# Kernel tuning notes

Hardware: AMD Instinct MI355X
Metric: run time of the kernel (lower is better)

The kernel has to match this reference:

```python
import jax, jax.numpy as jnp
import numpy as np

NQ = 4          # QUANTUM_QUBITS
DIM = 2 ** NQ   # 16-dim statevector
N_LAYERS = 2
BATCH = 1 << 20


def _bit(idx, w):
    # PennyLane convention: wire 0 is the most-significant bit
    return (idx >> (NQ - 1 - w)) & 1

# Precompute CNOT permutations for the ring (w, (w+1)%NQ): flip target bit when control bit is 1.
_CNOT_PERMS = []
for w in range(NQ):
    c, t = w, (w + 1) % NQ
    perm = np.arange(DIM)
    for idx in range(DIM):
        if _bit(idx, c):
            perm[idx] = idx ^ (1 << (NQ - 1 - t))
    _CNOT_PERMS.append(jnp.asarray(perm))

# Z expectation sign vectors: sign = +1 if bit==0 else -1, per wire -> (NQ, DIM)
_Z_SIGNS = jnp.asarray(
    np.stack([[1.0 - 2.0 * _bit(idx, w) for idx in range(DIM)] for w in range(NQ)]),
    dtype=jnp.float32,
)


def _ry(t):
    c, s = jnp.cos(t / 2), jnp.sin(t / 2)
    return jnp.stack([jnp.stack([c, -s], -1), jnp.stack([s, c], -1)], -2).astype(jnp.complex64)


def _rx(t):
    c = jnp.cos(t / 2).astype(jnp.complex64)
    s = (-1j * jnp.sin(t / 2)).astype(jnp.complex64)
    return jnp.stack([jnp.stack([c, s], -1), jnp.stack([s, c], -1)], -2)


def _rz(t):
    em = jnp.exp(-0.5j * t.astype(jnp.complex64))
    ep = jnp.exp(0.5j * t.astype(jnp.complex64))
    zero = jnp.zeros_like(em)
    return jnp.stack([jnp.stack([em, zero], -1), jnp.stack([zero, ep], -1)], -2)


def _apply_batched(state, g, w):
    # state: (B, DIM); g: (B, 2, 2) per-sample gate on wire w
    s = state.reshape((-1,) + (2,) * NQ)
    s = jnp.moveaxis(s, 1 + w, 1)
    s = jnp.einsum('bij,bj...->bi...', g, s)
    s = jnp.moveaxis(s, 1, 1 + w)
    return s.reshape(-1, DIM)


def _apply_shared(state, g, w):
    # state: (B, DIM); g: (2, 2) shared gate on wire w
    s = state.reshape((-1,) + (2,) * NQ)
    s = jnp.moveaxis(s, 1 + w, 1)
    s = jnp.einsum('ij,bj...->bi...', g, s)
    s = jnp.moveaxis(s, 1, 1 + w)
    return s.reshape(-1, DIM)


def setup_inputs() -> dict:
    key = jax.random.key(0)
    kx, kw = jax.random.split(key)
    x = jax.random.normal(kx, (BATCH, NQ), dtype=jnp.float32)
    weights = jax.random.normal(kw, (N_LAYERS, NQ, 3), dtype=jnp.float32) * 0.1
    return {"x": x, "weights": weights}


def reference(x, weights):
    B = x.shape[0]
    state = jnp.zeros((B, DIM), dtype=jnp.complex64).at[:, 0].set(1.0)
    # Angle embedding: RY(x_w) on each wire (per-sample gates)
    for w in range(NQ):
        state = _apply_batched(state, _ry(x[:, w]), w)
    # Variational layers: RX, RY, RZ per wire, then CNOT ring
    for l in range(weights.shape[0]):
        for w in range(NQ):
            state = _apply_shared(state, _rx(weights[l, w, 0]), w)
            state = _apply_shared(state, _ry(weights[l, w, 1]), w)
            state = _apply_shared(state, _rz(weights[l, w, 2]), w)
        for w in range(NQ):
            state = state[:, _CNOT_PERMS[w]]
    probs = (state.real ** 2 + state.imag ** 2)  # (B, DIM)
    return probs @ _Z_SIGNS.T  # (B, NQ) <Z_w> expvals
```

## Files before the change

### kernel.cpp

```cpp
#include <hip/hip_runtime.h>

#define NQ 4
#define DIM 16
#define NCOEF 136

struct cplx { float r, i; };
__device__ inline cplx cmul(cplx a, cplx b) { return {a.r*b.r - a.i*b.i, a.r*b.i + a.i*b.r}; }
__device__ inline cplx cadd(cplx a, cplx b) { return {a.r + b.r, a.i + b.i}; }

__global__ void setup_kernel(const float* __restrict__ wt, float* __restrict__ coef) {
    __shared__ float Ur[DIM][DIM];
    __shared__ float Ui[DIM][DIM];
    int col = threadIdx.x;
    if (col < DIM) {
        float ar[DIM], ai[DIM];
#pragma unroll
        for (int i = 0; i < DIM; ++i) { ar[i] = 0.f; ai[i] = 0.f; }
        ar[col] = 1.f;
        for (int l = 0; l < 2; ++l) {
            for (int q = 0; q < NQ; ++q) {
                float tx = wt[(l * 4 + q) * 3 + 0];
                float ty = wt[(l * 4 + q) * 3 + 1];
                float tz = wt[(l * 4 + q) * 3 + 2];
                float cx = cosf(0.5f * tx), sx = sinf(0.5f * tx);
                float cy = cosf(0.5f * ty), sy = sinf(0.5f * ty);
                float cz = cosf(0.5f * tz), sz = sinf(0.5f * tz);
                cplx Rx[2][2] = {{{cx, 0.f}, {0.f, -sx}}, {{0.f, -sx}, {cx, 0.f}}};
                cplx Ry[2][2] = {{{cy, 0.f}, {-sy, 0.f}}, {{sy, 0.f}, {cy, 0.f}}};
                cplx Rz[2][2] = {{{cz, -sz}, {0.f, 0.f}}, {{0.f, 0.f}, {cz, sz}}};
                cplx T[2][2], G[2][2];
                for (int r = 0; r < 2; ++r)
                    for (int c = 0; c < 2; ++c)
                        T[r][c] = cadd(cmul(Ry[r][0], Rx[0][c]), cmul(Ry[r][1], Rx[1][c]));
                for (int r = 0; r < 2; ++r)
                    for (int c = 0; c < 2; ++c)
                        G[r][c] = cadd(cmul(Rz[r][0], T[0][c]), cmul(Rz[r][1], T[1][c]));
                int pos = 3 - q, mask = 1 << pos;
                for (int idx = 0; idx < DIM; ++idx) {
                    if (idx & mask) continue;
                    int i1 = idx | mask;
                    cplx a0 = {ar[idx], ai[idx]}, a1 = {ar[i1], ai[i1]};
                    cplx n0 = cadd(cmul(G[0][0], a0), cmul(G[0][1], a1));
                    cplx n1 = cadd(cmul(G[1][0], a0), cmul(G[1][1], a1));
                    ar[idx] = n0.r; ai[idx] = n0.i;
                    ar[i1] = n1.r;  ai[i1] = n1.i;
                }
            }
            for (int q = 0; q < NQ; ++q) {
                int cpos = 3 - q, tpos = 3 - ((q + 1) & 3);
                int tmask = 1 << tpos;
                for (int idx = 0; idx < DIM; ++idx) {
                    if (((idx >> cpos) & 1) && !((idx >> tpos) & 1)) {
                        int i1 = idx | tmask;
                        float tr = ar[idx]; ar[idx] = ar[i1]; ar[i1] = tr;
                        float ti = ai[idx]; ai[idx] = ai[i1]; ai[i1] = ti;
                    }
                }
            }
        }
        for (int i = 0; i < DIM; ++i) { Ur[i][col] = ar[i]; Ui[i][col] = ai[i]; }
    }
    __syncthreads();
    for (int id = threadIdx.x; id < 4 * NCOEF; id += blockDim.x) {
        int u = id >> 2, wo = id & 3;
        int j = 0, rem = u;
        while (rem >= DIM - j) { rem -= DIM - j; ++j; }
        int k = j + rem;
        float acc = 0.f;
        for (int idx = 0; idx < DIM; ++idx) {
            float sgn = ((idx >> (3 - wo)) & 1) ? -1.f : 1.f;
            acc += sgn * (Ur[idx][j] * Ur[idx][k] + Ui[idx][j] * Ui[idx][k]);
        }
        coef[id] = (j == k) ? acc : 2.f * acc;
    }
}

__device__ inline void build_state(float4 xv, float* s) {
    float c0, s0, c1, s1, c2, s2, c3, s3;
    __sincosf(0.5f * xv.x, &s0, &c0);
    __sincosf(0.5f * xv.y, &s1, &c1);
    __sincosf(0.5f * xv.z, &s2, &c2);
    __sincosf(0.5f * xv.w, &s3, &c3);
    float p01[4] = {c0 * c1, c0 * s1, s0 * c1, s0 * s1};
    float p23[4] = {c2 * c3, c2 * s3, s2 * c3, s2 * s3};
#pragma unroll
    for (int a = 0; a < 4; ++a)
#pragma unroll
        for (int b = 0; b < 4; ++b)
            s[a * 4 + b] = p01[a] * p23[b];
}

__global__ __launch_bounds__(256) void qsim_kernel(const float4* __restrict__ x,
                                                   const float4* __restrict__ coef,
                                                   float4* __restrict__ out, int nthreads) {
    int tid = blockIdx.x * blockDim.x + threadIdx.x;
    if (tid >= nthreads) return;
    float4 xa = x[2 * tid + 0];
    float4 xb = x[2 * tid + 1];
    float sA[DIM], sB[DIM];
    build_state(xa, sA);
    build_state(xb, sB);
    float a0 = 0.f, a1 = 0.f, a2 = 0.f, a3 = 0.f;
    float b0 = 0.f, b1 = 0.f, b2 = 0.f, b3 = 0.f;
    int t = 0;
#pragma unroll
    for (int j = 0; j < DIM; ++j) {
#pragma unroll
        for (int k = j; k < DIM; ++k, ++t) {
            float4 c = coef[t];
            float pa = sA[j] * sA[k];
            float pb = sB[j] * sB[k];
            a0 = fmaf(c.x, pa, a0);
            a1 = fmaf(c.y, pa, a1);
            a2 = fmaf(c.z, pa, a2);
            a3 = fmaf(c.w, pa, a3);
            b0 = fmaf(c.x, pb, b0);
            b1 = fmaf(c.y, pb, b1);
            b2 = fmaf(c.z, pb, b2);
            b3 = fmaf(c.w, pb, b3);
        }
    }
    out[2 * tid + 0] = make_float4(a0, a1, a2, a3);
    out[2 * tid + 1] = make_float4(b0, b1, b2, b3);
}

extern "C" void kernel_launch(void* const* d_in, const int* in_sizes, int n_in,
                              void* d_out, int out_size, void* d_ws, size_t ws_size,
                              hipStream_t stream) {
    const float* x = (const float*)d_in[0];
    const float* wt = (const float*)d_in[1];
    float* out = (float*)d_out;
    float* coef = (float*)d_ws;

    setup_kernel<<<1, 256, 0, stream>>>(wt, coef);

    int B = in_sizes[0] / NQ;
    int nthreads = B / 2;
    int blocks = (nthreads + 255) / 256;
    qsim_kernel<<<blocks, 256, 0, stream>>>((const float4*)x, (const float4*)coef,
                                            (float4*)out, nthreads);
}
```

Before: 94.50 us.

## Re-express quadratic form in full-angle trig basis with 81 coefficients

The measurement is rewritten as a linear combination of products of 1, cos x and sin x per wire, using the full angle instead of the half angle. This needs 81 coefficients per output instead of 136 pairwise products. The setup kernel computes the per-wire observable matrices and Fourier-projects them into the new basis. The main kernel caches the coefficients in LDS and changes the batch split to tid and tid+half so loads stay coalesced. The intent is to cut FMA work and global constant loads per sample, at the cost of extra setup work and reliance on exact trig identities.

```diff
diff --git a/kernel.cpp b/kernel.cpp
--- a/kernel.cpp
+++ b/kernel.cpp
@@ -2,7 +2,6 @@
 
 #define NQ 4
 #define DIM 16
-#define NCOEF 136
 
 struct cplx { float r, i; };
 __device__ inline cplx cmul(cplx a, cplx b) { return {a.r*b.r - a.i*b.i, a.r*b.i + a.i*b.r}; }
@@ -11,6 +10,7 @@
 __global__ void setup_kernel(const float* __restrict__ wt, float* __restrict__ coef) {
     __shared__ float Ur[DIM][DIM];
     __shared__ float Ui[DIM][DIM];
+    __shared__ float A[4][DIM][DIM];
     int col = threadIdx.x;
     if (col < DIM) {
         float ar[DIM], ai[DIM];
@@ -61,67 +61,75 @@
         for (int i = 0; i < DIM; ++i) { Ur[i][col] = ar[i]; Ui[i][col] = ai[i]; }
     }
     __syncthreads();
-    for (int id = threadIdx.x; id < 4 * NCOEF; id += blockDim.x) {
-        int u = id >> 2, wo = id & 3;
-        int j = 0, rem = u;
-        while (rem >= DIM - j) { rem -= DIM - j; ++j; }
-        int k = j + rem;
+    for (int id = threadIdx.x; id < 4 * DIM * DIM; id += blockDim.x) {
+        int w = id >> 8, j = (id >> 4) & 15, k = id & 15;
         float acc = 0.f;
         for (int idx = 0; idx < DIM; ++idx) {
-            float sgn = ((idx >> (3 - wo)) & 1) ? -1.f : 1.f;
+            float sgn = ((idx >> (3 - w)) & 1) ? -1.f : 1.f;
             acc += sgn * (Ur[idx][j] * Ur[idx][k] + Ui[idx][j] * Ui[idx][k]);
         }
-        coef[id] = (j == k) ? acc : 2.f * acc;
+        A[w][j][k] = acc;
+    }
+    __syncthreads();
+    for (int id = threadIdx.x; id < 4 * 81; id += blockDim.x) {
+        int w = id & 3, u = id >> 2;
+        int e0 = u / 27, e1 = (u / 9) % 3, e2 = (u / 3) % 3, e3 = u % 3;
+        int m  = ((e0 == 2) ? 8 : 0) | ((e1 == 2) ? 4 : 0) | ((e2 == 2) ? 2 : 0) | ((e3 == 2) ? 1 : 0);
+        int d1 = ((e0 == 1) ? 8 : 0) | ((e1 == 1) ? 4 : 0) | ((e2 == 1) ? 2 : 0) | ((e3 == 1) ? 1 : 0);
+        float acc = 0.f;
+        for (int b = 0; b < DIM; ++b) {
+            float sgn = (__popc(b & d1) & 1) ? -1.f : 1.f;
+            acc += sgn * A[w][b][b ^ m];
+        }
+        coef[u * 4 + w] = 0.0625f * acc;
     }
 }
 
-__device__ inline void build_state(float4 xv, float* s) {
-    float c0, s0, c1, s1, c2, s2, c3, s3;
-    __sincosf(0.5f * xv.x, &s0, &c0);
-    __sincosf(0.5f * xv.y, &s1, &c1);
-    __sincosf(0.5f * xv.z, &s2, &c2);
-    __sincosf(0.5f * xv.w, &s3, &c3);
-    float p01[4] = {c0 * c1, c0 * s1, s0 * c1, s0 * s1};
-    float p23[4] = {c2 * c3, c2 * s3, s2 * c3, s2 * s3};
-#pragma unroll
-    for (int a = 0; a < 4; ++a)
-#pragma unroll
-        for (int b = 0; b < 4; ++b)
-            s[a * 4 + b] = p01[a] * p23[b];
+__device__ inline void build9(float u, float v, float* t) {
+    float su, cu, sv, cv;
+    __sincosf(u, &su, &cu);
+    __sincosf(v, &sv, &cv);
+    t[0] = 1.f;      t[1] = cv;      t[2] = sv;
+    t[3] = cu;       t[4] = cu * cv; t[5] = cu * sv;
+    t[6] = su;       t[7] = su * cv; t[8] = su * sv;
 }
 
 __global__ __launch_bounds__(256) void qsim_kernel(const float4* __restrict__ x,
                                                    const float4* __restrict__ coef,
-                                                   float4* __restrict__ out, int nthreads) {
+                                                   float4* __restrict__ out, int half) {
+    __shared__ float4 lk[81];
+    if (threadIdx.x < 81) lk[threadIdx.x] = coef[threadIdx.x];
+    __syncthreads();
+
     int tid = blockIdx.x * blockDim.x + threadIdx.x;
-    if (tid >= nthreads) return;
-    float4 xa = x[2 * tid + 0];
-    float4 xb = x[2 * tid + 1];
-    float sA[DIM], sB[DIM];
-    build_state(xa, sA);
-    build_state(xb, sB);
-    float a0 = 0.f, a1 = 0.f, a2 = 0.f, a3 = 0.f;
-    float b0 = 0.f, b1 = 0.f, b2 = 0.f, b3 = 0.f;
-    int t = 0;
+    if (tid >= half) return;
+    float4 xa = x[tid];
+    float4 xb = x[tid + half];
+    float ta[9], ua[9], tb[9], ub[9];
+    build9(xa.x, xa.y, ta);  build9(xa.z, xa.w, ua);
+    build9(xb.x, xb.y, tb);  build9(xb.z, xb.w, ub);
+
+    float4 accA = make_float4(0.f, 0.f, 0.f, 0.f);
+    float4 accB = make_float4(0.f, 0.f, 0.f, 0.f);
 #pragma unroll
-    for (int j = 0; j < DIM; ++j) {
+    for (int i = 0; i < 9; ++i) {
 #pragma unroll
-        for (int k = j; k < DIM; ++k, ++t) {
-            float4 c = coef[t];
-            float pa = sA[j] * sA[k];
-            float pb = sB[j] * sB[k];
-            a0 = fmaf(c.x, pa, a0);
-            a1 = fmaf(c.y, pa, a1);
-            a2 = fmaf(c.z, pa, a2);
-            a3 = fmaf(c.w, pa, a3);
-            b0 = fmaf(c.x, pb, b0);
-            b1 = fmaf(c.y, pb, b1);
-            b2 = fmaf(c.z, pb, b2);
-            b3 = fmaf(c.w, pb, b3);
+        for (int j = 0; j < 9; ++j) {
+            float4 c = lk[i * 9 + j];
+            float pa = ta[i] * ua[j];
+            float pb = tb[i] * ub[j];
+            accA.x = fmaf(c.x, pa, accA.x);
+            accA.y = fmaf(c.y, pa, accA.y);
+            accA.z = fmaf(c.z, pa, accA.z);
+            accA.w = fmaf(c.w, pa, accA.w);
+            accB.x = fmaf(c.x, pb, accB.x);
+            accB.y = fmaf(c.y, pb, accB.y);
+            accB.z = fmaf(c.z, pb, accB.z);
+            accB.w = fmaf(c.w, pb, accB.w);
         }
     }
-    out[2 * tid + 0] = make_float4(a0, a1, a2, a3);
-    out[2 * tid + 1] = make_float4(b0, b1, b2, b3);
+    out[tid] = accA;
+    out[tid + half] = accB;
 }
 
 extern "C" void kernel_launch(void* const* d_in, const int* in_sizes, int n_in,
@@ -135,8 +143,8 @@
     setup_kernel<<<1, 256, 0, stream>>>(wt, coef);
 
     int B = in_sizes[0] / NQ;
-    int nthreads = B / 2;
-    int blocks = (nthreads + 255) / 256;
+    int half = B / 2;
+    int blocks = (half + 255) / 256;
     qsim_kernel<<<blocks, 256, 0, stream>>>((const float4*)x, (const float4*)coef,
-                                            (float4*)out, nthreads);
+                                            (float4*)out, half);
 }
```

Result: faster. 91.13 us (-3.6%).
